# Kernel optimization log

Measured on AMD Instinct MI355X. Metric: run time of the kernel, lower is better.

Reference implementation:

```python
import jax, jax.numpy as jnp
import numpy as np

N, E, F_IN, H, L = 50000, 800000, 128, 256, 3


def setup_inputs() -> dict:
    key = jax.random.key(0)
    ks = jax.random.split(key, 6)
    s = 0.05  # keep activations well-scaled through 3 residual layers
    return {
        "x": jax.random.normal(ks[0], (N, F_IN), jnp.float32),
        "edge_index": jax.random.randint(ks[1], (2, E), 0, N, dtype=jnp.int32),
        "Wp": jax.random.normal(ks[2], (H, F_IN), jnp.float32) * s,
        "bp": jnp.zeros((H,), jnp.float32),
        "Wl": jax.random.normal(ks[3], (L, H, H), jnp.float32) * s,
        "bl": jnp.zeros((L, H), jnp.float32),
        "Wr": jax.random.normal(ks[4], (L, H, H), jnp.float32) * s,
        "gamma": jnp.ones((L, H), jnp.float32),
        "beta": jnp.zeros((L, H), jnp.float32),
    }


def _layernorm(x, g, b, eps=1e-5):
    mu = jnp.mean(x, axis=-1, keepdims=True)
    var = jnp.var(x, axis=-1, keepdims=True)
    return (x - mu) * jax.lax.rsqrt(var + eps) * g + b


def reference(x, edge_index, Wp, bp, Wl, bl, Wr, gamma, beta):
    n = x.shape[0]
    src, dst = edge_index[0], edge_index[1]
    # input projection + ReLU
    h = jax.nn.relu(x @ Wp.T + bp)  # [N, H]
    # mean-aggregation normalizer (PyG SAGEConv 'mean'): zero-degree nodes -> 0
    deg = jax.ops.segment_sum(jnp.ones_like(dst, jnp.float32), dst, num_segments=n)
    inv_deg = (1.0 / jnp.maximum(deg, 1.0))[:, None]  # [N, 1]
    num_layers = Wl.shape[0]
    for i in range(num_layers):
        res = h
        # SAGEConv: lin_l(mean of source-neighbor messages) + lin_r(self)
        agg = jax.ops.segment_sum(h[src], dst, num_segments=n) * inv_deg  # [N, H]
        h = agg @ Wl[i].T + bl[i] + h @ Wr[i].T
        # LayerNorm -> ReLU -> (dropout: eval-mode identity) -> residual
        h = jax.nn.relu(_layernorm(h, gamma[i], beta[i])) + res
    return h
```

## Files before the change

### kernel.cpp

```cpp
#include <hip/hip_runtime.h>

#define NN 50000
#define EE 800000
#define FIN 128
#define HH 256
#define NL 3

#define BM 64
#define BK 32
#define ABYTES (BM*BK*2)
#define BBYTES (HH*BK*2)
#define TILEB  (ABYTES + BBYTES)

typedef __bf16 bf16x8 __attribute__((ext_vector_type(8)));
typedef float  f32x4  __attribute__((ext_vector_type(4)));
typedef unsigned short u16x8 __attribute__((ext_vector_type(8)));

__device__ __forceinline__ float bf2f(unsigned short u){
    union { unsigned int i; float f; } v; v.i = ((unsigned int)u) << 16; return v.f;
}
__device__ __forceinline__ unsigned short f2bf(float f){
    union { float f; unsigned int i; } v; v.f = f;
    unsigned int r = v.i + 0x7FFF + ((v.i >> 16) & 1);
    return (unsigned short)(r >> 16);
}
__device__ __forceinline__ void gload16(const void* g, void* s){
    __builtin_amdgcn_global_load_lds(
        (const __attribute__((address_space(1))) void*)g,
        (__attribute__((address_space(3))) void*)s, 16, 0, 0);
}

__global__ void k_zero_i32(int* __restrict__ p, int n){
    int i = blockIdx.x*256 + threadIdx.x;
    if (i < n) p[i] = 0;
}
__global__ void k_count_deg(const int* __restrict__ dst, int* __restrict__ deg){
    int i = blockIdx.x*256 + threadIdx.x;
    if (i < EE) atomicAdd(&deg[dst[i]], 1);
}
__global__ void k_block_sum(const int* __restrict__ deg, int* __restrict__ bsum){
    __shared__ int s[1024];
    int i = blockIdx.x*1024 + threadIdx.x;
    s[threadIdx.x] = (i < NN) ? deg[i] : 0;
    __syncthreads();
    for (int o = 512; o > 0; o >>= 1){
        if (threadIdx.x < o) s[threadIdx.x] += s[threadIdx.x + o];
        __syncthreads();
    }
    if (threadIdx.x == 0) bsum[blockIdx.x] = s[0];
}
__global__ void k_scan_bsum(int* __restrict__ bsum, int nb){
    if (threadIdx.x == 0 && blockIdx.x == 0){
        int run = 0;
        for (int i = 0; i < nb; ++i){ int v = bsum[i]; bsum[i] = run; run += v; }
    }
}
__global__ void k_make_off(const int* __restrict__ deg, const int* __restrict__ bsum,
                           int* __restrict__ off, int* __restrict__ pos,
                           float* __restrict__ invd){
    __shared__ int s[1024];
    int t = threadIdx.x;
    int i = blockIdx.x*1024 + t;
    int v = (i < NN) ? deg[i] : 0;
    s[t] = v; __syncthreads();
    for (int o = 1; o < 1024; o <<= 1){
        int add = (t >= o) ? s[t - o] : 0;
        __syncthreads();
        s[t] += add;
        __syncthreads();
    }
    if (i < NN){
        int excl = s[t] - v + bsum[blockIdx.x];
        off[i] = excl; pos[i] = excl;
        invd[i] = 1.0f / fmaxf((float)v, 1.0f);
    }
}
__global__ void k_build_csr(const int* __restrict__ src, const int* __restrict__ dst,
                            int* __restrict__ pos, int* __restrict__ csr){
    int i = blockIdx.x*256 + threadIdx.x;
    if (i < EE){
        int p = atomicAdd(&pos[dst[i]], 1);
        csr[p] = src[i];
    }
}

#define NX  (NN*FIN/4)
#define NWP (HH*FIN/4)
#define NWC (NL*HH*2*HH/4)
__global__ void k_prep(const float* __restrict__ x, const float* __restrict__ Wp,
                       const float* __restrict__ Wl, const float* __restrict__ Wr,
                       unsigned short* __restrict__ Xb, unsigned short* __restrict__ Wpb,
                       unsigned short* __restrict__ Wb){
    int i = blockIdx.x*256 + threadIdx.x;
    if (i < NX){
        float4 v = *(const float4*)&x[i*4];
        ushort4 o; o.x=f2bf(v.x); o.y=f2bf(v.y); o.z=f2bf(v.z); o.w=f2bf(v.w);
        *(ushort4*)&Xb[i*4] = o;
        return;
    }
    int j = i - NX;
    if (j < NWP){
        float4 v = *(const float4*)&Wp[j*4];
        ushort4 o; o.x=f2bf(v.x); o.y=f2bf(v.y); o.z=f2bf(v.z); o.w=f2bf(v.w);
        *(ushort4*)&Wpb[j*4] = o;
        return;
    }
    int k4 = j - NWP;
    if (k4 < NWC){
        int base = k4*4;
        int kk  = base & 511;
        int n   = (base >> 9) & (HH-1);
        int lyr = base >> 17;
        const float* srcp = (kk < HH) ? &Wl[((size_t)lyr*HH + n)*HH + kk]
                                      : &Wr[((size_t)lyr*HH + n)*HH + (kk - HH)];
        float4 v = *(const float4*)srcp;
        ushort4 o; o.x=f2bf(v.x); o.y=f2bf(v.y); o.z=f2bf(v.z); o.w=f2bf(v.w);
        *(ushort4*)&Wb[base] = o;
    }
}

__device__ __forceinline__ void accum16(float* a, uint4 v, float c){
    const unsigned int w0 = v.x, w1 = v.y, w2 = v.z, w3 = v.w;
    #pragma unroll
    for (int b = 0; b < 4; ++b){
        a[b]    += c * (float)((w0 >> (8*b)) & 0xFF);
        a[4+b]  += c * (float)((w1 >> (8*b)) & 0xFF);
        a[8+b]  += c * (float)((w2 >> (8*b)) & 0xFF);
        a[12+b] += c * (float)((w3 >> (8*b)) & 0xFF);
    }
}

__global__ __launch_bounds__(256) void k_aggregate_u8(
    const unsigned char* __restrict__ hu, const float* __restrict__ scl,
    const int* __restrict__ csr, const int* __restrict__ off,
    const int* __restrict__ deg, const float* __restrict__ invd,
    unsigned short* __restrict__ aggb)
{
    const int wave = threadIdx.x >> 6, lane = threadIdx.x & 63;
    const int node = blockIdx.x*4 + wave;
    if (node >= NN) return;
    const int o = off[node], d = deg[node];
    const int grp = lane >> 4;
    const int fl  = lane & 15;

    float acc[16] = {};
    int j = 0;
    for (; j + 16 <= d; j += 16){
        int s0 = csr[o + j      + grp];
        int s1 = csr[o + j + 4  + grp];
        int s2 = csr[o + j + 8  + grp];
        int s3 = csr[o + j + 12 + grp];
        float c0 = scl[s0], c1 = scl[s1], c2 = scl[s2], c3 = scl[s3];
        uint4 v0 = *(const uint4*)&hu[(size_t)s0*HH + fl*16];
        uint4 v1 = *(const uint4*)&hu[(size_t)s1*HH + fl*16];
        uint4 v2 = *(const uint4*)&hu[(size_t)s2*HH + fl*16];
        uint4 v3 = *(const uint4*)&hu[(size_t)s3*HH + fl*16];
        accum16(acc, v0, c0); accum16(acc, v1, c1);
        accum16(acc, v2, c2); accum16(acc, v3, c3);
    }
    for (; j + 8 <= d; j += 8){
        int s0 = csr[o + j     + grp];
        int s1 = csr[o + j + 4 + grp];
        float c0 = scl[s0], c1 = scl[s1];
        uint4 v0 = *(const uint4*)&hu[(size_t)s0*HH + fl*16];
        uint4 v1 = *(const uint4*)&hu[(size_t)s1*HH + fl*16];
        accum16(acc, v0, c0); accum16(acc, v1, c1);
    }
    for (; j < d; j += 4){
        int idx = j + grp;
        int s0 = 0; float c0 = 0.f;
        if (idx < d){ s0 = csr[o + idx]; c0 = scl[s0]; }
        uint4 v0 = *(const uint4*)&hu[(size_t)s0*HH + fl*16];
        accum16(acc, v0, c0);
    }
    #pragma unroll
    for (int k = 0; k < 16; ++k){
        acc[k] += __shfl_xor(acc[k], 16);
        acc[k] += __shfl_xor(acc[k], 32);
    }
    if (grp == 0){
        float id = invd[node];
        u16x8 r0, r1;
        #pragma unroll
        for (int k = 0; k < 8; ++k){
            r0[k] = f2bf(acc[k]*id);
            r1[k] = f2bf(acc[8+k]*id);
        }
        *(u16x8*)&aggb[(size_t)node*HH + fl*16]     = r0;
        *(u16x8*)&aggb[(size_t)node*HH + fl*16 + 8] = r1;
    }
}

template<int EPI>
__global__ __launch_bounds__(512) void k_gemm_mfma(
    const unsigned short* __restrict__ A0, int lda0,
    const unsigned short* __restrict__ A1, int lda1,
    const unsigned short* __restrict__ Bt,
    const float* __restrict__ bias,
    const float* __restrict__ gamma, const float* __restrict__ beta,
    const unsigned short* __restrict__ resb,
    float* __restrict__ outf, unsigned short* __restrict__ outb,
    unsigned char* __restrict__ hu, float* __restrict__ scl,
    int K0, int KTOT)
{
    __shared__ char smem[2*TILEB];
    const int t  = threadIdx.x;
    const int w  = t >> 6, l = t & 63;
    const int lr = l & 15, lg = l >> 4;
    const int wm = w >> 2, wn = w & 3;
    const int m0 = blockIdx.x * BM;

    const char* bsrc[2]; int bdst[2];
    #pragma unroll
    for (int i = 0; i < 2; ++i){
        int u   = t + i*512;
        int row = u >> 2;
        int swz = ((u & 3)*16) ^ ((row & 6) << 3);
        bsrc[i] = (const char*)(Bt + (size_t)row*KTOT) + swz;
        bdst[i] = ABYTES + u*16;
    }
    const int ua   = t & 255;
    const int rowA = ua >> 2;
    const int swzA = ((ua & 3)*16) ^ ((rowA & 6) << 3);
    int growA = m0 + rowA; if (growA > NN-1) growA = NN-1;
    const char* a0src = (const char*)(A0 + (size_t)growA*lda0) + swzA;
    const char* a1src = (const char*)(A1 + (size_t)growA*lda1) + swzA;
    const int adst = ua*16;
    const bool hasA = (w < 4);

    f32x4 acc[2][4] = {};

    auto stage = [&](int s, int buf){
        const int k0 = s * BK;
        char* dst = smem + buf*TILEB;
        if (hasA){
            const char* g = (k0 < K0) ? (a0src + (size_t)k0*2)
                                      : (a1src + (size_t)(k0 - K0)*2);
            gload16(g, dst + adst);
        }
        gload16(bsrc[0] + (size_t)k0*2, dst + bdst[0]);
        gload16(bsrc[1] + (size_t)k0*2, dst + bdst[1]);
    };

    const int nsteps = KTOT / BK;
    stage(0, 0);
    for (int s = 0; s < nsteps; ++s){
        const int cur = s & 1;
        if (s + 1 < nsteps){
            stage(s + 1, cur ^ 1);
            if (hasA) { asm volatile("s_waitcnt vmcnt(3)" ::: "memory"); }
            else      { asm volatile("s_waitcnt vmcnt(2)" ::: "memory"); }
        } else {
            asm volatile("s_waitcnt vmcnt(0)" ::: "memory");
        }
        __builtin_amdgcn_s_barrier();
        __builtin_amdgcn_sched_barrier(0);

        const char* As = smem + cur*TILEB;
        const char* Bs = As + ABYTES;
        const int kb = lg * 16;
        const int sw = (lr & 6) << 3;
        bf16x8 af[2], bfr[4];
        #pragma unroll
        for (int m = 0; m < 2; ++m){
            int r = wm*32 + m*16 + lr;
            af[m] = *(const bf16x8*)(As + r*64 + (kb ^ sw));
        }
        #pragma unroll
        for (int n = 0; n < 4; ++n){
            int r = wn*64 + n*16 + lr;
            bfr[n] = *(const bf16x8*)(Bs + r*64 + (kb ^ sw));
        }
        #pragma unroll
        for (int m = 0; m < 2; ++m)
            #pragma unroll
            for (int n = 0; n < 4; ++n)
                acc[m][n] = __builtin_amdgcn_mfma_f32_16x16x32_bf16(af[m], bfr[n], acc[m][n], 0, 0, 0);

        asm volatile("s_waitcnt lgkmcnt(0)" ::: "memory");
        __builtin_amdgcn_s_barrier();
    }

    float bcol[4], gcol[4], becol[4];
    #pragma unroll
    for (int n = 0; n < 4; ++n){
        int c = wn*64 + n*16 + lr;
        bcol[n] = bias[c];
        if (EPI >= 1){ gcol[n] = gamma[c]; becol[n] = beta[c]; }
    }

    float* red  = (float*)smem;
    float* red2 = red + 512;
    float pmx[2][4];

    if (EPI == 0){
        #pragma unroll
        for (int m = 0; m < 2; ++m)
        #pragma unroll
        for (int reg = 0; reg < 4; ++reg){
            int R = wm*32 + m*16 + lg*4 + reg;
            int grow = m0 + R;
            float mx = 0.f;
            #pragma unroll
            for (int n = 0; n < 4; ++n){
                int c = wn*64 + n*16 + lr;
                float v = fmaxf(acc[m][n][reg] + bcol[n], 0.f);
                acc[m][n][reg] = v;
                mx = fmaxf(mx, v);
                if (grow < NN) outb[(size_t)grow*HH + c] = f2bf(v);
            }
            pmx[m][reg] = mx;
        }
    } else {
        float sm[2][4], sq[2][4];
        #pragma unroll
        for (int m = 0; m < 2; ++m)
        #pragma unroll
        for (int reg = 0; reg < 4; ++reg){
            float s = 0.f, q = 0.f;
            #pragma unroll
            for (int n = 0; n < 4; ++n){
                float v = acc[m][n][reg] + bcol[n];
                acc[m][n][reg] = v;
                s += v; q += v*v;
            }
            sm[m][reg] = s; sq[m][reg] = q;
        }
        #pragma unroll
        for (int mask = 1; mask <= 8; mask <<= 1){
            #pragma unroll
            for (int m = 0; m < 2; ++m)
            #pragma unroll
            for (int reg = 0; reg < 4; ++reg){
                sm[m][reg] += __shfl_xor(sm[m][reg], mask);
                sq[m][reg] += __shfl_xor(sq[m][reg], mask);
            }
        }
        if (lr == 0){
            #pragma unroll
            for (int m = 0; m < 2; ++m)
            #pragma unroll
            for (int reg = 0; reg < 4; ++reg){
                int R = wm*32 + m*16 + lg*4 + reg;
                red[(wn*64 + R)*2 + 0] = sm[m][reg];
                red[(wn*64 + R)*2 + 1] = sq[m][reg];
            }
        }
        __syncthreads();
        #pragma unroll
        for (int m = 0; m < 2; ++m)
        #pragma unroll
        for (int reg = 0; reg < 4; ++reg){
            int R = wm*32 + m*16 + lg*4 + reg;
            float S = 0.f, Q = 0.f;
            #pragma unroll
            for (int ww = 0; ww < 4; ++ww){
                S += red[(ww*64 + R)*2 + 0];
                Q += red[(ww*64 + R)*2 + 1];
            }
            float mean = S * (1.0f/HH);
            float var  = Q * (1.0f/HH) - mean*mean;
            float inv  = rsqrtf(var + 1e-5f);
            int grow = m0 + R;
            int growc = (grow > NN-1) ? NN-1 : grow;
            float mx = 0.f;
            #pragma unroll
            for (int n = 0; n < 4; ++n){
                int c = wn*64 + n*16 + lr;
                float o = fmaxf((acc[m][n][reg] - mean)*inv*gcol[n] + becol[n], 0.f)
                          + bf2f(resb[(size_t)growc*HH + c]);
                acc[m][n][reg] = o;
                mx = fmaxf(mx, o);
                if (grow < NN){
                    if (EPI == 1) outb[(size_t)grow*HH + c] = f2bf(o);
                    else          outf[(size_t)grow*HH + c] = o;
                }
            }
            pmx[m][reg] = mx;
        }
    }

    if (EPI <= 1){
        #pragma unroll
        for (int mask = 1; mask <= 8; mask <<= 1){
            #pragma unroll
            for (int m = 0; m < 2; ++m)
            #pragma unroll
            for (int reg = 0; reg < 4; ++reg)
                pmx[m][reg] = fmaxf(pmx[m][reg], __shfl_xor(pmx[m][reg], mask));
        }
        if (lr == 0){
            #pragma unroll
            for (int m = 0; m < 2; ++m)
            #pragma unroll
            for (int reg = 0; reg < 4; ++reg){
                int R = wm*32 + m*16 + lg*4 + reg;
                red2[wn*64 + R] = pmx[m][reg];
            }
        }
        __syncthreads();
        #pragma unroll
        for (int m = 0; m < 2; ++m)
        #pragma unroll
        for (int reg = 0; reg < 4; ++reg){
            int R = wm*32 + m*16 + lg*4 + reg;
            float rmax = fmaxf(fmaxf(red2[R], red2[64 + R]),
                               fmaxf(red2[128 + R], red2[192 + R]));
            float qinv = (rmax > 0.f) ? (255.0f / rmax) : 0.f;
            int grow = m0 + R;
            if (grow >= NN) continue;
            #pragma unroll
            for (int n = 0; n < 4; ++n){
                int c = wn*64 + n*16 + lr;
                hu[(size_t)grow*HH + c] = (unsigned char)(acc[m][n][reg]*qinv + 0.5f);
            }
            if (wn == 0 && lr == 0) scl[grow] = rmax * (1.0f/255.0f);
        }
    }
}

extern "C" void kernel_launch(void* const* d_in, const int* in_sizes, int n_in,
                              void* d_out, int out_size, void* d_ws, size_t ws_size,
                              hipStream_t stream) {
    const float* x     = (const float*)d_in[0];
    const int*   ei    = (const int*)d_in[1];
    const int*   srcI  = ei;
    const int*   dstI  = ei + EE;
    const float* Wp    = (const float*)d_in[2];
    const float* bp    = (const float*)d_in[3];
    const float* Wl    = (const float*)d_in[4];
    const float* bl    = (const float*)d_in[5];
    const float* Wr    = (const float*)d_in[6];
    const float* gamma = (const float*)d_in[7];
    const float* beta  = (const float*)d_in[8];
    float* out = (float*)d_out;

    char* ws = (char*)d_ws;
    size_t off_b = 0;
    auto alloc = [&](size_t bytes) -> char* {
        char* p = ws + off_b;
        off_b = (off_b + bytes + 255) & ~(size_t)255;
        return p;
    };
    unsigned short* Hb0  = (unsigned short*)alloc((size_t)NN*HH*2);
    unsigned short* Hb1  = (unsigned short*)alloc((size_t)NN*HH*2);
    unsigned short* AGGb = (unsigned short*)alloc((size_t)NN*HH*2);
    unsigned char*  Hu0  = (unsigned char*)alloc((size_t)NN*HH);
    unsigned char*  Hu1  = (unsigned char*)alloc((size_t)NN*HH);
    float* Scl0 = (float*)alloc((size_t)NN*4);
    float* Scl1 = (float*)alloc((size_t)NN*4);
    unsigned short* Xb = (unsigned short*)alloc((size_t)NN*FIN*2);
    int*   csr  = (int*)alloc((size_t)EE*4);
    int*   deg  = (int*)alloc((size_t)NN*4);
    int*   offs = (int*)alloc((size_t)NN*4);
    int*   pos  = (int*)alloc((size_t)NN*4);
    float* invd = (float*)alloc((size_t)NN*4);
    int*   bsum = (int*)alloc(64*4);
    unsigned short* Wpb = (unsigned short*)alloc((size_t)HH*FIN*2);
    unsigned short* Wb  = (unsigned short*)alloc((size_t)NL*HH*2*HH*2);
    (void)ws_size; (void)in_sizes; (void)n_in; (void)out_size;

    const int NB = (NN + 1023)/1024;

    k_zero_i32<<<(NN + 255)/256, 256, 0, stream>>>(deg, NN);
    k_count_deg<<<(EE + 255)/256, 256, 0, stream>>>(dstI, deg);
    k_block_sum<<<NB, 1024, 0, stream>>>(deg, bsum);
    k_scan_bsum<<<1, 1, 0, stream>>>(bsum, NB);
    k_make_off<<<NB, 1024, 0, stream>>>(deg, bsum, offs, pos, invd);
    k_build_csr<<<(EE + 255)/256, 256, 0, stream>>>(srcI, dstI, pos, csr);

    k_prep<<<(NX + NWP + NWC + 255)/256, 256, 0, stream>>>(x, Wp, Wl, Wr, Xb, Wpb, Wb);

    const int GB = (NN + BM - 1)/BM;

    k_gemm_mfma<0><<<GB, 512, 0, stream>>>(Xb, FIN, Xb, FIN, Wpb, bp,
                                           nullptr, nullptr, nullptr,
                                           nullptr, Hb0, Hu0, Scl0,
                                           FIN, FIN);

    unsigned short* hin = Hb0;
    unsigned char*  huin = Hu0;
    float*          sclin = Scl0;
    for (int lyr = 0; lyr < NL; ++lyr){
        k_aggregate_u8<<<(NN + 3)/4, 256, 0, stream>>>(huin, sclin, csr, offs, deg,
                                                       invd, AGGb);
        unsigned short* hout  = (hin == Hb0) ? Hb1 : Hb0;
        unsigned char*  huout = (huin == Hu0) ? Hu1 : Hu0;
        float*          sclout= (sclin == Scl0) ? Scl1 : Scl0;
        const unsigned short* Wbt = Wb + (size_t)lyr*HH*2*HH;
        if (lyr < NL-1)
            k_gemm_mfma<1><<<GB, 512, 0, stream>>>(AGGb, HH, hin, HH, Wbt, bl + lyr*HH,
                                                   gamma + lyr*HH, beta + lyr*HH, hin,
                                                   nullptr, hout, huout, sclout,
                                                   HH, 2*HH);
        else
            k_gemm_mfma<2><<<GB, 512, 0, stream>>>(AGGb, HH, hin, HH, Wbt, bl + lyr*HH,
                                                   gamma + lyr*HH, beta + lyr*HH, hin,
                                                   out, nullptr, nullptr, nullptr,
                                                   HH, 2*HH);
        hin = hout; huin = huout; sclin = sclout;
    }
}
```

Baseline: 376.3 us.

## Load GEMM A operand directly from global and stage B in 128-wide K chunks

```diff
diff --git a/kernel.cpp b/kernel.cpp
--- a/kernel.cpp
+++ b/kernel.cpp
@@ -7,10 +7,6 @@
 #define NL 3
 
 #define BM 64
-#define BK 32
-#define ABYTES (BM*BK*2)
-#define BBYTES (HH*BK*2)
-#define TILEB  (ABYTES + BBYTES)
 
 typedef __bf16 bf16x8 __attribute__((ext_vector_type(8)));
 typedef float  f32x4  __attribute__((ext_vector_type(4)));
@@ -191,7 +187,7 @@
     }
 }
 
-template<int EPI>
+template<int EPI, int K0, int KTOT>
 __global__ __launch_bounds__(512) void k_gemm_mfma(
     const unsigned short* __restrict__ A0, int lda0,
     const unsigned short* __restrict__ A1, int lda1,
@@ -200,86 +196,80 @@
     const float* __restrict__ gamma, const float* __restrict__ beta,
     const unsigned short* __restrict__ resb,
     float* __restrict__ outf, unsigned short* __restrict__ outb,
-    unsigned char* __restrict__ hu, float* __restrict__ scl,
-    int K0, int KTOT)
+    unsigned char* __restrict__ hu, float* __restrict__ scl)
 {
-    __shared__ char smem[2*TILEB];
+    __shared__ char smem[65536];
     const int t  = threadIdx.x;
     const int w  = t >> 6, l = t & 63;
     const int lr = l & 15, lg = l >> 4;
     const int wm = w >> 2, wn = w & 3;
     const int m0 = blockIdx.x * BM;
-
-    const char* bsrc[2]; int bdst[2];
-    #pragma unroll
-    for (int i = 0; i < 2; ++i){
-        int u   = t + i*512;
-        int row = u >> 2;
-        int swz = ((u & 3)*16) ^ ((row & 6) << 3);
-        bsrc[i] = (const char*)(Bt + (size_t)row*KTOT) + swz;
-        bdst[i] = ABYTES + u*16;
-    }
-    const int ua   = t & 255;
-    const int rowA = ua >> 2;
-    const int swzA = ((ua & 3)*16) ^ ((rowA & 6) << 3);
-    int growA = m0 + rowA; if (growA > NN-1) growA = NN-1;
-    const char* a0src = (const char*)(A0 + (size_t)growA*lda0) + swzA;
-    const char* a1src = (const char*)(A1 + (size_t)growA*lda1) + swzA;
-    const int adst = ua*16;
-    const bool hasA = (w < 4);
+    constexpr int NQ = KTOT / 128;
+
+    const char* bsrc[8]; int bdst[8];
+    #pragma unroll
+    for (int i = 0; i < 8; ++i){
+        int u   = i*512 + t;
+        int row = u >> 4;
+        int c   = u & 15;
+        bsrc[i] = (const char*)(Bt + (size_t)row*KTOT) + ((c ^ (row & 7))*16);
+        bdst[i] = u*16;
+    }
+    auto stage = [&](int q){
+        #pragma unroll
+        for (int i = 0; i < 8; ++i)
+            gload16(bsrc[i] + q*256, smem + bdst[i]);
+    };
+
+    int arow[2];
+    #pragma unroll
+    for (int m = 0; m < 2; ++m){
+        int r = m0 + wm*32 + m*16 + lr;
+        arow[m] = (r > NN-1) ? NN-1 : r;
+    }
+    int brow[4];
+    #pragma unroll
+    for (int n = 0; n < 4; ++n) brow[n] = (wn*64 + n*16 + lr)*256;
+    const int sx = lr & 7;
 
     f32x4 acc[2][4] = {};
 
-    auto stage = [&](int s, int buf){
-        const int k0 = s * BK;
-        char* dst = smem + buf*TILEB;
-        if (hasA){
-            const char* g = (k0 < K0) ? (a0src + (size_t)k0*2)
-                                      : (a1src + (size_t)(k0 - K0)*2);
-            gload16(g, dst + adst);
-        }
-        gload16(bsrc[0] + (size_t)k0*2, dst + bdst[0]);
-        gload16(bsrc[1] + (size_t)k0*2, dst + bdst[1]);
-    };
-
-    const int nsteps = KTOT / BK;
-    stage(0, 0);
-    for (int s = 0; s < nsteps; ++s){
-        const int cur = s & 1;
-        if (s + 1 < nsteps){
-            stage(s + 1, cur ^ 1);
-            if (hasA) { asm volatile("s_waitcnt vmcnt(3)" ::: "memory"); }
-            else      { asm volatile("s_waitcnt vmcnt(2)" ::: "memory"); }
-        } else {
-            asm volatile("s_waitcnt vmcnt(0)" ::: "memory");
-        }
-        __builtin_amdgcn_s_barrier();
-        __builtin_amdgcn_sched_barrier(0);
-
-        const char* As = smem + cur*TILEB;
-        const char* Bs = As + ABYTES;
-        const int kb = lg * 16;
-        const int sw = (lr & 6) << 3;
-        bf16x8 af[2], bfr[4];
-        #pragma unroll
-        for (int m = 0; m < 2; ++m){
-            int r = wm*32 + m*16 + lr;
-            af[m] = *(const bf16x8*)(As + r*64 + (kb ^ sw));
-        }
-        #pragma unroll
-        for (int n = 0; n < 4; ++n){
-            int r = wn*64 + n*16 + lr;
-            bfr[n] = *(const bf16x8*)(Bs + r*64 + (kb ^ sw));
-        }
-        #pragma unroll
-        for (int m = 0; m < 2; ++m)
+    stage(0);
+    __syncthreads();
+
+    #pragma unroll 1
+    for (int q = 0; q < NQ; ++q){
+        const int kg = q*128;
+        const unsigned short* Ap;
+        int ldap;
+        if (kg < K0){ Ap = A0 + kg + lg*8; ldap = lda0; }
+        else        { Ap = A1 + (kg - K0) + lg*8; ldap = lda1; }
+
+        #pragma unroll
+        for (int s = 0; s < 4; ++s){
+            bf16x8 af[2], bfr[4];
+            #pragma unroll
+            for (int m = 0; m < 2; ++m)
+                af[m] = *(const bf16x8*)(Ap + (size_t)arow[m]*ldap + s*32);
             #pragma unroll
             for (int n = 0; n < 4; ++n)
-                acc[m][n] = __builtin_amdgcn_mfma_f32_16x16x32_bf16(af[m], bfr[n], acc[m][n], 0, 0, 0);
-
-        asm volatile("s_waitcnt lgkmcnt(0)" ::: "memory");
-        __builtin_amdgcn_s_barrier();
-    }
+                bfr[n] = *(const bf16x8*)(smem + brow[n] + (((s*4 + lg) ^ sx) << 4));
+            __builtin_amdgcn_s_setprio(1);
+            #pragma unroll
+            for (int m = 0; m < 2; ++m)
+                #pragma unroll
+                for (int n = 0; n < 4; ++n)
+                    acc[m][n] = __builtin_amdgcn_mfma_f32_16x16x32_bf16(af[m], bfr[n], acc[m][n], 0, 0, 0);
+            __builtin_amdgcn_s_setprio(0);
+        }
+
+        if (q + 1 < NQ){
+            __syncthreads();
+            stage(q + 1);
+            __syncthreads();
+        }
+    }
+    __syncthreads();
 
     float bcol[4], gcol[4], becol[4];
     #pragma unroll
@@ -473,10 +463,9 @@
 
     const int GB = (NN + BM - 1)/BM;
 
-    k_gemm_mfma<0><<<GB, 512, 0, stream>>>(Xb, FIN, Xb, FIN, Wpb, bp,
-                                           nullptr, nullptr, nullptr,
-                                           nullptr, Hb0, Hu0, Scl0,
-                                           FIN, FIN);
+    k_gemm_mfma<0,128,128><<<GB, 512, 0, stream>>>(Xb, FIN, Xb, FIN, Wpb, bp,
+                                                   nullptr, nullptr, nullptr,
+                                                   nullptr, Hb0, Hu0, Scl0);
 
     unsigned short* hin = Hb0;
     unsigned char*  huin = Hu0;
@@ -489,15 +478,13 @@
         float*          sclout= (sclin == Scl0) ? Scl1 : Scl0;
         const unsigned short* Wbt = Wb + (size_t)lyr*HH*2*HH;
         if (lyr < NL-1)
-            k_gemm_mfma<1><<<GB, 512, 0, stream>>>(AGGb, HH, hin, HH, Wbt, bl + lyr*HH,
-                                                   gamma + lyr*HH, beta + lyr*HH, hin,
-                                                   nullptr, hout, huout, sclout,
-                                                   HH, 2*HH);
+            k_gemm_mfma<1,256,512><<<GB, 512, 0, stream>>>(AGGb, HH, hin, HH, Wbt, bl + lyr*HH,
+                                                           gamma + lyr*HH, beta + lyr*HH, hin,
+                                                           nullptr, hout, huout, sclout);
         else
-            k_gemm_mfma<2><<<GB, 512, 0, stream>>>(AGGb, HH, hin, HH, Wbt, bl + lyr*HH,
-                                                   gamma + lyr*HH, beta + lyr*HH, hin,
-                                                   out, nullptr, nullptr, nullptr,
-                                                   HH, 2*HH);
+            k_gemm_mfma<2,256,512><<<GB, 512, 0, stream>>>(AGGb, HH, hin, HH, Wbt, bl + lyr*HH,
+                                                           gamma + lyr*HH, beta + lyr*HH, hin,
+                                                           out, nullptr, nullptr, nullptr);
         hin = hout; huin = huout; sclin = sclout;
     }
 }
```

New measurement: 408.9 us. 8.7% more time.

## Stage GEMM epilogue through LDS for coalesced vector stores; fuse block-sum scan

Applied to the files above, without the earlier changes.

```diff
diff --git a/kernel.cpp b/kernel.cpp
--- a/kernel.cpp
+++ b/kernel.cpp
@@ -11,6 +11,10 @@
 #define ABYTES (BM*BK*2)
 #define BBYTES (HH*BK*2)
 #define TILEB  (ABYTES + BBYTES)
+
+#define STG_S 280
+#define QST_S 272
+#define FST_S 268
 
 typedef __bf16 bf16x8 __attribute__((ext_vector_type(8)));
 typedef float  f32x4  __attribute__((ext_vector_type(4)));
@@ -49,20 +53,21 @@
     }
     if (threadIdx.x == 0) bsum[blockIdx.x] = s[0];
 }
-__global__ void k_scan_bsum(int* __restrict__ bsum, int nb){
-    if (threadIdx.x == 0 && blockIdx.x == 0){
-        int run = 0;
-        for (int i = 0; i < nb; ++i){ int v = bsum[i]; bsum[i] = run; run += v; }
-    }
-}
 __global__ void k_make_off(const int* __restrict__ deg, const int* __restrict__ bsum,
-                           int* __restrict__ off, int* __restrict__ pos,
+                           int nb, int* __restrict__ off, int* __restrict__ pos,
                            float* __restrict__ invd){
     __shared__ int s[1024];
+    __shared__ int base;
     int t = threadIdx.x;
+    if (t < 64){
+        int v = (t < blockIdx.x && t < nb) ? bsum[t] : 0;
+        #pragma unroll
+        for (int m = 1; m <= 32; m <<= 1) v += __shfl_xor(v, m);
+        if (t == 0) base = v;
+    }
     int i = blockIdx.x*1024 + t;
-    int v = (i < NN) ? deg[i] : 0;
-    s[t] = v; __syncthreads();
+    int v0 = (i < NN) ? deg[i] : 0;
+    s[t] = v0; __syncthreads();
     for (int o = 1; o < 1024; o <<= 1){
         int add = (t >= o) ? s[t - o] : 0;
         __syncthreads();
@@ -70,9 +75,9 @@
         __syncthreads();
     }
     if (i < NN){
-        int excl = s[t] - v + bsum[blockIdx.x];
+        int excl = s[t] - v0 + base;
         off[i] = excl; pos[i] = excl;
-        invd[i] = 1.0f / fmaxf((float)v, 1.0f);
+        invd[i] = 1.0f / fmaxf((float)v0, 1.0f);
     }
 }
 __global__ void k_build_csr(const int* __restrict__ src, const int* __restrict__ dst,
@@ -291,15 +296,88 @@
 
     float* red  = (float*)smem;
     float* red2 = red + 512;
+    unsigned short* stg = (unsigned short*)(smem + 4096);
+    unsigned char*  qst = (unsigned char*)(smem + 4096);
+    float*          fst = (float*)(smem + 4096);
     float pmx[2][4];
 
-    if (EPI == 0){
+    if (EPI >= 1){
+        #pragma unroll
+        for (int i = 0; i < 4; ++i){
+            int c16 = t + i*512;
+            int row = c16 >> 5;
+            int cc  = (c16 & 31) * 8;
+            int grow = m0 + row; if (grow > NN-1) grow = NN-1;
+            u16x8 rv = *(const u16x8*)&resb[(size_t)grow*HH + cc];
+            *(u16x8*)&stg[row*STG_S + cc] = rv;
+        }
+        float sm[2][4], sq[2][4];
+        #pragma unroll
+        for (int m = 0; m < 2; ++m)
+        #pragma unroll
+        for (int reg = 0; reg < 4; ++reg){
+            float s = 0.f, q = 0.f;
+            #pragma unroll
+            for (int n = 0; n < 4; ++n){
+                float v = acc[m][n][reg] + bcol[n];
+                acc[m][n][reg] = v;
+                s += v; q += v*v;
+            }
+            sm[m][reg] = s; sq[m][reg] = q;
+        }
+        #pragma unroll
+        for (int mask = 1; mask <= 8; mask <<= 1){
+            #pragma unroll
+            for (int m = 0; m < 2; ++m)
+            #pragma unroll
+            for (int reg = 0; reg < 4; ++reg){
+                sm[m][reg] += __shfl_xor(sm[m][reg], mask);
+                sq[m][reg] += __shfl_xor(sq[m][reg], mask);
+            }
+        }
+        if (lr == 0){
+            #pragma unroll
+            for (int m = 0; m < 2; ++m)
+            #pragma unroll
+            for (int reg = 0; reg < 4; ++reg){
+                int R = wm*32 + m*16 + lg*4 + reg;
+                red[(wn*64 + R)*2 + 0] = sm[m][reg];
+                red[(wn*64 + R)*2 + 1] = sq[m][reg];
+            }
+        }
+        __syncthreads();
         #pragma unroll
         for (int m = 0; m < 2; ++m)
         #pragma unroll
         for (int reg = 0; reg < 4; ++reg){
             int R = wm*32 + m*16 + lg*4 + reg;
-            int grow = m0 + R;
+            float S = 0.f, Q = 0.f;
+            #pragma unroll
+            for (int ww = 0; ww < 4; ++ww){
+                S += red[(ww*64 + R)*2 + 0];
+                Q += red[(ww*64 + R)*2 + 1];
+            }
+            float mean = S * (1.0f/HH);
+            float var  = Q * (1.0f/HH) - mean*mean;
+            float inv  = rsqrtf(var + 1e-5f);
+            float mx = 0.f;
+            #pragma unroll
+            for (int n = 0; n < 4; ++n){
+                int c = wn*64 + n*16 + lr;
+                float o = fmaxf((acc[m][n][reg] - mean)*inv*gcol[n] + becol[n], 0.f)
+                          + bf2f(stg[R*STG_S + c]);
+                acc[m][n][reg] = o;
+                mx = fmaxf(mx, o);
+                if (EPI == 1) stg[R*STG_S + c] = f2bf(o);
+            }
+            pmx[m][reg] = mx;
+        }
+    } else {
+        #pragma unroll
+        for (int m = 0; m < 2; ++m)
+        #pragma unroll
+        for (int reg = 0; reg < 4; ++reg){
+            int R = wm*32 + m*16 + lg*4 + reg;
             float mx = 0.f;
             #pragma unroll
             for (int n = 0; n < 4; ++n){
@@ -307,74 +385,7 @@
                 float v = fmaxf(acc[m][n][reg] + bcol[n], 0.f);
                 acc[m][n][reg] = v;
                 mx = fmaxf(mx, v);
-                if (grow < NN) outb[(size_t)grow*HH + c] = f2bf(v);
-            }
-            pmx[m][reg] = mx;
-        }
-    } else {
-        float sm[2][4], sq[2][4];
-        #pragma unroll
-        for (int m = 0; m < 2; ++m)
-        #pragma unroll
-        for (int reg = 0; reg < 4; ++reg){
-            float s = 0.f, q = 0.f;
-            #pragma unroll
-            for (int n = 0; n < 4; ++n){
-                float v = acc[m][n][reg] + bcol[n];
-                acc[m][n][reg] = v;
-                s += v; q += v*v;
-            }
-            sm[m][reg] = s; sq[m][reg] = q;
-        }
-        #pragma unroll
-        for (int mask = 1; mask <= 8; mask <<= 1){
-            #pragma unroll
-            for (int m = 0; m < 2; ++m)
-            #pragma unroll
-            for (int reg = 0; reg < 4; ++reg){
-                sm[m][reg] += __shfl_xor(sm[m][reg], mask);
-                sq[m][reg] += __shfl_xor(sq[m][reg], mask);
-            }
-        }
-        if (lr == 0){
-            #pragma unroll
-            for (int m = 0; m < 2; ++m)
-            #pragma unroll
-            for (int reg = 0; reg < 4; ++reg){
-                int R = wm*32 + m*16 + lg*4 + reg;
-                red[(wn*64 + R)*2 + 0] = sm[m][reg];
-                red[(wn*64 + R)*2 + 1] = sq[m][reg];
-            }
-        }
-        __syncthreads();
-        #pragma unroll
-        for (int m = 0; m < 2; ++m)
-        #pragma unroll
-        for (int reg = 0; reg < 4; ++reg){
-            int R = wm*32 + m*16 + lg*4 + reg;
-            float S = 0.f, Q = 0.f;
-            #pragma unroll
-            for (int ww = 0; ww < 4; ++ww){
-                S += red[(ww*64 + R)*2 + 0];
-                Q += red[(ww*64 + R)*2 + 1];
-            }
-            float mean = S * (1.0f/HH);
-            float var  = Q * (1.0f/HH) - mean*mean;
-            float inv  = rsqrtf(var + 1e-5f);
-            int grow = m0 + R;
-            int growc = (grow > NN-1) ? NN-1 : grow;
-            float mx = 0.f;
-            #pragma unroll
-            for (int n = 0; n < 4; ++n){
-                int c = wn*64 + n*16 + lr;
-                float o = fmaxf((acc[m][n][reg] - mean)*inv*gcol[n] + becol[n], 0.f)
-                          + bf2f(resb[(size_t)growc*HH + c]);
-                acc[m][n][reg] = o;
-                mx = fmaxf(mx, o);
-                if (grow < NN){
-                    if (EPI == 1) outb[(size_t)grow*HH + c] = f2bf(o);
-                    else          outf[(size_t)grow*HH + c] = o;
-                }
+                stg[R*STG_S + c] = f2bf(v);
             }
             pmx[m][reg] = mx;
         }
@@ -399,6 +410,20 @@
             }
         }
         __syncthreads();
+
+        #pragma unroll
+        for (int i = 0; i < 4; ++i){
+            int c16 = t + i*512;
+            int row = c16 >> 5;
+            int cc  = (c16 & 31) * 8;
+            int grow = m0 + row;
+            if (grow < NN){
+                u16x8 v = *(const u16x8*)&stg[row*STG_S + cc];
+                *(u16x8*)&outb[(size_t)grow*HH + cc] = v;
+            }
+        }
+        __syncthreads();
+
         #pragma unroll
         for (int m = 0; m < 2; ++m)
         #pragma unroll
@@ -407,14 +432,56 @@
             float rmax = fmaxf(fmaxf(red2[R], red2[64 + R]),
                                fmaxf(red2[128 + R], red2[192 + R]));
             float qinv = (rmax > 0.f) ? (255.0f / rmax) : 0.f;
-            int grow = m0 + R;
-            if (grow >= NN) continue;
             #pragma unroll
             for (int n = 0; n < 4; ++n){
                 int c = wn*64 + n*16 + lr;
-                hu[(size_t)grow*HH + c] = (unsigned char)(acc[m][n][reg]*qinv + 0.5f);
-            }
-            if (wn == 0 && lr == 0) scl[grow] = rmax * (1.0f/255.0f);
+                qst[R*QST_S + c] = (unsigned char)(acc[m][n][reg]*qinv + 0.5f);
+            }
+            if (wn == 0 && lr == 0 && m0 + R < NN) scl[m0 + R] = rmax * (1.0f/255.0f);
+        }
+        __syncthreads();
+
+        #pragma unroll
+        for (int i = 0; i < 2; ++i){
+            int c16 = t + i*512;
+            int row = c16 >> 4;
+            int cc  = (c16 & 15) * 16;
+            int grow = m0 + row;
+            if (grow < NN){
+                uint4 v = *(const uint4*)&qst[row*QST_S + cc];
+                *(uint4*)&hu[(size_t)grow*HH + cc] = v;
+            }
+        }
+    } else {
+        __syncthreads();
+        #pragma unroll
+        for (int half = 0; half < 2; ++half){
+            if (wm == half){
+                #pragma unroll
+                for (int m = 0; m < 2; ++m)
+                #pragma unroll
+                for (int reg = 0; reg < 4; ++reg){
+                    int R32 = m*16 + lg*4 + reg;
+                    #pragma unroll
+                    for (int n = 0; n < 4; ++n){
+                        int c = wn*64 + n*16 + lr;
+                        fst[R32*FST_S + c] = acc[m][n][reg];
+                    }
+                }
+            }
+            __syncthreads();
+            #pragma unroll
+            for (int i = 0; i < 4; ++i){
+                int c16 = t + i*512;
+                int row = c16 >> 6;
+                int cc  = (c16 & 63) * 4;
+                int grow = m0 + half*32 + row;
+                if (grow < NN){
+                    f32x4 v = *(const f32x4*)&fst[row*FST_S + cc];
+                    *(f32x4*)&outf[(size_t)grow*HH + cc] = v;
+                }
+            }
+            __syncthreads();
         }
     }
 }
@@ -465,8 +532,7 @@
     k_zero_i32<<<(NN + 255)/256, 256, 0, stream>>>(deg, NN);
     k_count_deg<<<(EE + 255)/256, 256, 0, stream>>>(dstI, deg);
     k_block_sum<<<NB, 1024, 0, stream>>>(deg, bsum);
-    k_scan_bsum<<<1, 1, 0, stream>>>(bsum, NB);
-    k_make_off<<<NB, 1024, 0, stream>>>(deg, bsum, offs, pos, invd);
+    k_make_off<<<NB, 1024, 0, stream>>>(deg, bsum, NB, offs, pos, invd);
     k_build_csr<<<(EE + 255)/256, 256, 0, stream>>>(srcI, dstI, pos, csr);
 
     k_prep<<<(NX + NWP + NWC + 255)/256, 256, 0, stream>>>(x, Wp, Wl, Wr, Xb, Wpb, Wb);
```

New measurement: 364.9 us. 1.03x faster.

## Fuse CSR build into projection GEMM, merge scan, and vectorize epilogue stores

Applied to the files above, without the earlier changes.

```diff
diff --git a/kernel.cpp b/kernel.cpp
--- a/kernel.cpp
+++ b/kernel.cpp
@@ -11,6 +11,7 @@
 #define ABYTES (BM*BK*2)
 #define BBYTES (HH*BK*2)
 #define TILEB  (ABYTES + BBYTES)
+#define CSRB   782
 
 typedef __bf16 bf16x8 __attribute__((ext_vector_type(8)));
 typedef float  f32x4  __attribute__((ext_vector_type(4)));
@@ -28,6 +29,9 @@
     __builtin_amdgcn_global_load_lds(
         (const __attribute__((address_space(1))) void*)g,
         (__attribute__((address_space(3))) void*)s, 16, 0, 0);
+}
+__device__ __forceinline__ int permslot(int n){
+    return (n & ~63) | ((n & 3) << 4) | ((n >> 2) & 15);
 }
 
 __global__ void k_zero_i32(int* __restrict__ p, int n){
@@ -49,20 +53,21 @@
     }
     if (threadIdx.x == 0) bsum[blockIdx.x] = s[0];
 }
-__global__ void k_scan_bsum(int* __restrict__ bsum, int nb){
-    if (threadIdx.x == 0 && blockIdx.x == 0){
-        int run = 0;
-        for (int i = 0; i < nb; ++i){ int v = bsum[i]; bsum[i] = run; run += v; }
-    }
-}
 __global__ void k_make_off(const int* __restrict__ deg, const int* __restrict__ bsum,
-                           int* __restrict__ off, int* __restrict__ pos,
+                           int nb, int* __restrict__ off, int* __restrict__ pos,
                            float* __restrict__ invd){
     __shared__ int s[1024];
+    __shared__ int base;
     int t = threadIdx.x;
+    if (t < 64){
+        int v = (t < blockIdx.x && t < nb) ? bsum[t] : 0;
+        #pragma unroll
+        for (int m = 1; m <= 32; m <<= 1) v += __shfl_xor(v, m);
+        if (t == 0) base = v;
+    }
     int i = blockIdx.x*1024 + t;
-    int v = (i < NN) ? deg[i] : 0;
-    s[t] = v; __syncthreads();
+    int v0 = (i < NN) ? deg[i] : 0;
+    s[t] = v0; __syncthreads();
     for (int o = 1; o < 1024; o <<= 1){
         int add = (t >= o) ? s[t - o] : 0;
         __syncthreads();
@@ -70,17 +75,9 @@
         __syncthreads();
     }
     if (i < NN){
-        int excl = s[t] - v + bsum[blockIdx.x];
+        int excl = s[t] - v0 + base;
         off[i] = excl; pos[i] = excl;
-        invd[i] = 1.0f / fmaxf((float)v, 1.0f);
-    }
-}
-__global__ void k_build_csr(const int* __restrict__ src, const int* __restrict__ dst,
-                            int* __restrict__ pos, int* __restrict__ csr){
-    int i = blockIdx.x*256 + threadIdx.x;
-    if (i < EE){
-        int p = atomicAdd(&pos[dst[i]], 1);
-        csr[p] = src[i];
+        invd[i] = 1.0f / fmaxf((float)v0, 1.0f);
     }
 }
 
@@ -100,9 +97,12 @@
     }
     int j = i - NX;
     if (j < NWP){
-        float4 v = *(const float4*)&Wp[j*4];
+        int base = j*4;
+        int kk = base & (FIN-1);
+        int n  = base >> 7;
+        float4 v = *(const float4*)&Wp[base];
         ushort4 o; o.x=f2bf(v.x); o.y=f2bf(v.y); o.z=f2bf(v.z); o.w=f2bf(v.w);
-        *(ushort4*)&Wpb[j*4] = o;
+        *(ushort4*)&Wpb[permslot(n)*FIN + kk] = o;
         return;
     }
     int k4 = j - NWP;
@@ -115,7 +115,7 @@
                                       : &Wr[((size_t)lyr*HH + n)*HH + (kk - HH)];
         float4 v = *(const float4*)srcp;
         ushort4 o; o.x=f2bf(v.x); o.y=f2bf(v.y); o.z=f2bf(v.z); o.w=f2bf(v.w);
-        *(ushort4*)&Wb[base] = o;
+        *(ushort4*)&Wb[(size_t)lyr*HH*2*HH + permslot(n)*2*HH + kk] = o;
     }
 }
 
@@ -191,7 +191,7 @@
     }
 }
 
-template<int EPI>
+template<int EPI, bool CSR>
 __global__ __launch_bounds__(512) void k_gemm_mfma(
     const unsigned short* __restrict__ A0, int lda0,
     const unsigned short* __restrict__ A1, int lda1,
@@ -201,9 +201,20 @@
     const unsigned short* __restrict__ resb,
     float* __restrict__ outf, unsigned short* __restrict__ outb,
     unsigned char* __restrict__ hu, float* __restrict__ scl,
-    int K0, int KTOT)
+    int K0, int KTOT, int ngemm,
+    const int* __restrict__ esrc, const int* __restrict__ edst,
+    int* __restrict__ pos, int* __restrict__ csr)
 {
     __shared__ char smem[2*TILEB];
+    if (CSR && (int)blockIdx.x >= ngemm){
+        int i = ((int)blockIdx.x - ngemm)*512 + (int)threadIdx.x;
+        const int stride = CSRB*512;
+        for (; i < EE; i += stride){
+            int p = atomicAdd(&pos[edst[i]], 1);
+            csr[p] = esrc[i];
+        }
+        return;
+    }
     const int t  = threadIdx.x;
     const int w  = t >> 6, l = t & 63;
     const int lr = l & 15, lg = l >> 4;
@@ -281,12 +292,15 @@
         __builtin_amdgcn_s_barrier();
     }
 
-    float bcol[4], gcol[4], becol[4];
-    #pragma unroll
-    for (int n = 0; n < 4; ++n){
-        int c = wn*64 + n*16 + lr;
-        bcol[n] = bias[c];
-        if (EPI >= 1){ gcol[n] = gamma[c]; becol[n] = beta[c]; }
+    const int cb = wn*64 + lr*4;
+    float4 bq = *(const float4*)&bias[cb];
+    float bcol[4] = {bq.x, bq.y, bq.z, bq.w};
+    float gcol[4], becol[4];
+    if (EPI >= 1){
+        float4 gq = *(const float4*)&gamma[cb];
+        float4 eq = *(const float4*)&beta[cb];
+        gcol[0]=gq.x; gcol[1]=gq.y; gcol[2]=gq.z; gcol[3]=gq.w;
+        becol[0]=eq.x; becol[1]=eq.y; becol[2]=eq.z; becol[3]=eq.w;
     }
 
     float* red  = (float*)smem;
@@ -301,14 +315,15 @@
             int R = wm*32 + m*16 + lg*4 + reg;
             int grow = m0 + R;
             float mx = 0.f;
+            ushort4 hb4;
             #pragma unroll
             for (int n = 0; n < 4; ++n){
-                int c = wn*64 + n*16 + lr;
                 float v = fmaxf(acc[m][n][reg] + bcol[n], 0.f);
                 acc[m][n][reg] = v;
                 mx = fmaxf(mx, v);
-                if (grow < NN) outb[(size_t)grow*HH + c] = f2bf(v);
-            }
+                ((unsigned short*)&hb4)[n] = f2bf(v);
+            }
+            if (grow < NN) *(ushort4*)&outb[(size_t)grow*HH + cb] = hb4;
             pmx[m][reg] = mx;
         }
     } else {
@@ -363,18 +378,22 @@
             float inv  = rsqrtf(var + 1e-5f);
             int grow = m0 + R;
             int growc = (grow > NN-1) ? NN-1 : grow;
+            ushort4 rv = *(const ushort4*)&resb[(size_t)growc*HH + cb];
             float mx = 0.f;
+            ushort4 hb4;
+            f32x4 fo;
             #pragma unroll
             for (int n = 0; n < 4; ++n){
-                int c = wn*64 + n*16 + lr;
                 float o = fmaxf((acc[m][n][reg] - mean)*inv*gcol[n] + becol[n], 0.f)
-                          + bf2f(resb[(size_t)growc*HH + c]);
+                          + bf2f(((const unsigned short*)&rv)[n]);
                 acc[m][n][reg] = o;
                 mx = fmaxf(mx, o);
-                if (grow < NN){
-                    if (EPI == 1) outb[(size_t)grow*HH + c] = f2bf(o);
-                    else          outf[(size_t)grow*HH + c] = o;
-                }
+                if (EPI == 1) ((unsigned short*)&hb4)[n] = f2bf(o);
+                else          fo[n] = o;
+            }
+            if (grow < NN){
+                if (EPI == 1) *(ushort4*)&outb[(size_t)grow*HH + cb] = hb4;
+                else          *(f32x4*)&outf[(size_t)grow*HH + cb] = fo;
             }
             pmx[m][reg] = mx;
         }
@@ -389,6 +408,7 @@
             for (int reg = 0; reg < 4; ++reg)
                 pmx[m][reg] = fmaxf(pmx[m][reg], __shfl_xor(pmx[m][reg], mask));
         }
+        if (EPI == 0) __syncthreads();
         if (lr == 0){
             #pragma unroll
             for (int m = 0; m < 2; ++m)
@@ -409,11 +429,13 @@
             float qinv = (rmax > 0.f) ? (255.0f / rmax) : 0.f;
             int grow = m0 + R;
             if (grow >= NN) continue;
+            unsigned int q4 = 0;
             #pragma unroll
             for (int n = 0; n < 4; ++n){
-                int c = wn*64 + n*16 + lr;
-                hu[(size_t)grow*HH + c] = (unsigned char)(acc[m][n][reg]*qinv + 0.5f);
-            }
+                unsigned int qv = (unsigned int)(acc[m][n][reg]*qinv + 0.5f);
+                q4 |= qv << (8*n);
+            }
+            *(unsigned int*)&hu[(size_t)grow*HH + cb] = q4;
             if (wn == 0 && lr == 0) scl[grow] = rmax * (1.0f/255.0f);
         }
     }
@@ -465,18 +487,16 @@
     k_zero_i32<<<(NN + 255)/256, 256, 0, stream>>>(deg, NN);
     k_count_deg<<<(EE + 255)/256, 256, 0, stream>>>(dstI, deg);
     k_block_sum<<<NB, 1024, 0, stream>>>(deg, bsum);
-    k_scan_bsum<<<1, 1, 0, stream>>>(bsum, NB);
-    k_make_off<<<NB, 1024, 0, stream>>>(deg, bsum, offs, pos, invd);
-    k_build_csr<<<(EE + 255)/256, 256, 0, stream>>>(srcI, dstI, pos, csr);
-
     k_prep<<<(NX + NWP + NWC + 255)/256, 256, 0, stream>>>(x, Wp, Wl, Wr, Xb, Wpb, Wb);
+    k_make_off<<<NB, 1024, 0, stream>>>(deg, bsum, NB, offs, pos, invd);
 
     const int GB = (NN + BM - 1)/BM;
 
-    k_gemm_mfma<0><<<GB, 512, 0, stream>>>(Xb, FIN, Xb, FIN, Wpb, bp,
-                                           nullptr, nullptr, nullptr,
-                                           nullptr, Hb0, Hu0, Scl0,
-                                           FIN, FIN);
+    k_gemm_mfma<0,true><<<GB + CSRB, 512, 0, stream>>>(
+        Xb, FIN, Xb, FIN, Wpb, bp,
+        nullptr, nullptr, nullptr,
+        nullptr, Hb0, Hu0, Scl0,
+        FIN, FIN, GB, srcI, dstI, pos, csr);
 
     unsigned short* hin = Hb0;
     unsigned char*  huin = Hu0;
@@ -489,15 +509,17 @@
         float*          sclout= (sclin == Scl0) ? Scl1 : Scl0;
         const unsigned short* Wbt = Wb + (size_t)lyr*HH*2*HH;
         if (lyr < NL-1)
-            k_gemm_mfma<1><<<GB, 512, 0, stream>>>(AGGb, HH, hin, HH, Wbt, bl + lyr*HH,
-                                                   gamma + lyr*HH, beta + lyr*HH, hin,
-                                                   nullptr, hout, huout, sclout,
-                                                   HH, 2*HH);
+            k_gemm_mfma<1,false><<<GB, 512, 0, stream>>>(
+                AGGb, HH, hin, HH, Wbt, bl + lyr*HH,
+                gamma + lyr*HH, beta + lyr*HH, hin,
+                nullptr, hout, huout, sclout,
+                HH, 2*HH, GB, nullptr, nullptr, nullptr, nullptr);
         else
-            k_gemm_mfma<2><<<GB, 512, 0, stream>>>(AGGb, HH, hin, HH, Wbt, bl + lyr*HH,
-                                                   gamma + lyr*HH, beta + lyr*HH, hin,
-                                                   out, nullptr, nullptr, nullptr,
-                                                   HH, 2*HH);
+            k_gemm_mfma<2,false><<<GB, 512, 0, stream>>>(
+                AGGb, HH, hin, HH, Wbt, bl + lyr*HH,
+                gamma + lyr*HH, beta + lyr*HH, hin,
+                out, nullptr, nullptr, nullptr,
+                HH, 2*HH, GB, nullptr, nullptr, nullptr, nullptr);
         hin = hout; huin = huout; sclin = sclout;
     }
 }
```

New measurement: 370.2 us. Within noise of the previous version (-1.6%).
